# Kernel tuning notes

Measured on AMD Instinct MI355X. Metric: run time of the kernel, lower is better.

Reference implementation:

```python
import jax, jax.numpy as jnp
import numpy as np

N = 50000   # nodes
E = 800000  # edges (avg degree 16)
C = 96      # in = hidden = out channels


def setup_inputs() -> dict:
    key = jax.random.key(0)
    ks = jax.random.split(key, 8)
    s = np.float32(1.0 / np.sqrt(C))
    x = jax.random.normal(ks[0], (N, C), dtype=jnp.float32)
    edge_index = jax.random.randint(ks[1], (2, E), 0, N, dtype=jnp.int64)
    W1 = jax.random.normal(ks[2], (C, C), dtype=jnp.float32) * s
    Wr1 = jax.random.normal(ks[3], (C, C), dtype=jnp.float32) * s
    b1 = jnp.zeros((C,), dtype=jnp.float32)
    W2 = jax.random.normal(ks[4], (C, C), dtype=jnp.float32) * s
    Wr2 = jax.random.normal(ks[5], (C, C), dtype=jnp.float32) * s
    b2 = jnp.zeros((C,), dtype=jnp.float32)
    return {"x": x, "edge_index": edge_index,
            "W1": W1, "Wr1": Wr1, "b1": b1,
            "W2": W2, "Wr2": Wr2, "b2": b2}


def spline_conv(x, edge_index, W, W_root, b):
    """Gather-transform-scatter message passing (SplineConv core, mean aggr)."""
    src, dst = edge_index[0], edge_index[1]
    h = x @ W                                   # [N, C] transform once per node
    msg = h[src]                                # [E, C] edge gather
    agg = jax.ops.segment_sum(msg, dst, num_segments=N)        # scatter-add
    deg = jax.ops.segment_sum(jnp.ones((E,), x.dtype), dst, num_segments=N)
    agg = agg / jnp.maximum(deg, 1.0)[:, None]  # mean aggregation
    return agg + x @ W_root + b                 # root weight + bias


def reference(x, edge_index, W1, Wr1, b1, W2, Wr2, b2):
    h = jax.nn.relu(spline_conv(x, edge_index, W1, Wr1, b1))
    out = spline_conv(h, edge_index, W2, Wr2, b2)
    return out.reshape(-1)  # generalization of x.view(1600)
```

## Files before the change

### kernel.cpp

```cpp
#include <hip/hip_runtime.h>

#define C 96
#define TB 64
#define EB 2048
#define NBP 1024
#define LCAP 2048
#define F8S 128
typedef unsigned char u8;
typedef unsigned short u16;
typedef unsigned int u32;
typedef __attribute__((ext_vector_type(8))) short short8;
typedef __attribute__((ext_vector_type(4))) float floatx4;
typedef __attribute__((ext_vector_type(2))) float floatx2;

__device__ inline u16 f2bf(float f) {
    union { float f; u32 u; } v; v.f = f;
    u32 r = v.u + 0x7fff + ((v.u >> 16) & 1);
    return (u16)(r >> 16);
}
__device__ inline u32 pk4_fp8(float a, float b, float c, float d) {
    u32 w = 0;
    w = __builtin_amdgcn_cvt_pk_fp8_f32(a, b, w, false);
    w = __builtin_amdgcn_cvt_pk_fp8_f32(c, d, w, true);
    return w;
}
__device__ inline u8 f2fp8(float a) {
    return (u8)(__builtin_amdgcn_cvt_pk_fp8_f32(a, a, 0, false) & 0xff);
}

__global__ __launch_bounds__(256) void sort_kernel(const int* __restrict__ src,
                                                   const int* __restrict__ dst,
                                                   u32* __restrict__ tabT,
                                                   u32* __restrict__ stage,
                                                   int E, int DB, int NB,
                                                   const float* __restrict__ x,
                                                   u16* __restrict__ xb,
                                                   u8* __restrict__ xf8, int n16, int CX,
                                                   const float* W0, const float* W1,
                                                   const float* W2, const float* W3,
                                                   u16* T0, u16* T1, u16* T2, u16* T3) {
    int bid = blockIdx.x;
    int t = threadIdx.x;
    if (bid >= DB) {
        int cc = bid - DB;
        if (cc < CX) {
            int i = cc * 256 + t;
            if (i >= n16) return;
            const float4* p = (const float4*)x + (size_t)i * 4;
            float4 a = p[0], b = p[1], c = p[2], d = p[3];
            short8 o0, o1;
            o0[0] = (short)f2bf(a.x); o0[1] = (short)f2bf(a.y);
            o0[2] = (short)f2bf(a.z); o0[3] = (short)f2bf(a.w);
            o0[4] = (short)f2bf(b.x); o0[5] = (short)f2bf(b.y);
            o0[6] = (short)f2bf(b.z); o0[7] = (short)f2bf(b.w);
            o1[0] = (short)f2bf(c.x); o1[1] = (short)f2bf(c.y);
            o1[2] = (short)f2bf(c.z); o1[3] = (short)f2bf(c.w);
            o1[4] = (short)f2bf(d.x); o1[5] = (short)f2bf(d.y);
            o1[6] = (short)f2bf(d.z); o1[7] = (short)f2bf(d.w);
            *(short8*)(xb + (size_t)i * 16) = o0;
            *(short8*)(xb + (size_t)i * 16 + 8) = o1;
            uint4 f8;
            f8.x = pk4_fp8(a.x, a.y, a.z, a.w);
            f8.y = pk4_fp8(b.x, b.y, b.z, b.w);
            f8.z = pk4_fp8(c.x, c.y, c.z, c.w);
            f8.w = pk4_fp8(d.x, d.y, d.z, d.w);
            int node = i / 6, slice = i - node * 6;
            *(uint4*)(xf8 + (size_t)node * F8S + slice * 16) = f8;
        } else {
            int w = cc - CX;
            const float* W = w == 0 ? W0 : w == 1 ? W1 : w == 2 ? W2 : W3;
            u16* T = w == 0 ? T0 : w == 1 ? T1 : w == 2 ? T2 : T3;
            for (int i = t; i < C * C; i += 256) {
                int k = i / C, n = i - k * C;
                T[n * C + k] = f2bf(W[i]);
            }
        }
        return;
    }

    __shared__ u32 s_word[EB];
    __shared__ int s_cnt[NBP];
    __shared__ int s_off[NBP];
    __shared__ int s_scan[256];
    int e0 = bid * EB;
    int cnt_here = min(EB, E - e0);

    for (int i = t; i < NBP; i += 256) s_cnt[i] = 0;
    __syncthreads();

    int my_src[EB / 256], my_dl[EB / 256], my_b[EB / 256], my_rank[EB / 256];
    int nmine = 0;
#pragma unroll
    for (int k = 0; k < EB / 256; k++) {
        int i = t + k * 256;
        if (i < cnt_here) {
            int s = src[e0 + i], d = dst[e0 + i];
            int b = d >> 6;
            my_src[nmine] = s;
            my_dl[nmine] = d & (TB - 1);
            my_b[nmine] = b;
            my_rank[nmine] = atomicAdd(&s_cnt[b], 1);
            nmine++;
        }
    }
    __syncthreads();

    int b4 = t * 4;
    int v0 = s_cnt[b4], v1 = s_cnt[b4 + 1], v2 = s_cnt[b4 + 2], v3 = s_cnt[b4 + 3];
    int lsum = v0 + v1 + v2 + v3;
    s_scan[t] = lsum;
    __syncthreads();
    for (int off = 1; off < 256; off <<= 1) {
        int x2 = (t >= off) ? s_scan[t - off] : 0;
        __syncthreads();
        s_scan[t] += x2;
        __syncthreads();
    }
    int excl = s_scan[t] - lsum;
    s_off[b4] = excl;
    s_off[b4 + 1] = excl + v0;
    s_off[b4 + 2] = excl + v0 + v1;
    s_off[b4 + 3] = excl + v0 + v1 + v2;
    __syncthreads();

    for (int b = t; b < NB; b += 256)
        tabT[(size_t)b * DB + bid] = ((u32)s_cnt[b] << 16) | (u32)s_off[b];

    for (int k = 0; k < nmine; k++) {
        int slot = s_off[my_b[k]] + my_rank[k];
        s_word[slot] = ((u32)my_dl[k] << 16) | (u32)my_src[k];
    }
    __syncthreads();

    for (int i = t; i < cnt_here; i += 256) stage[(size_t)bid * EB + i] = s_word[i];
}

template <bool RELU, bool WF8, typename OT>
__global__ __launch_bounds__(256, 4) void layer_kernel(const u16* __restrict__ Xbf,
                                                       const u8* __restrict__ Xf8,
                                                       const u32* __restrict__ tabT,
                                                       const u32* __restrict__ stage,
                                                       const u16* __restrict__ WTA,
                                                       const u16* __restrict__ WTR,
                                                       const float* __restrict__ BIAS,
                                                       OT* __restrict__ Y,
                                                       u8* __restrict__ Yf8, int n, int DB) {
    __shared__ __align__(16) u16 sA[64 * 104];
    __shared__ u16 lcsr[LCAP];
    __shared__ int s_dg[TB];
    __shared__ int s_off64[TB];
    __shared__ int s_cur64[TB];
    __shared__ int s_perm[TB];
    __shared__ int ssum[256];
    u32* raw = (u32*)sA;
    const int t = threadIdx.x;
    const int b = blockIdx.x;
    const int row0 = b * 64;
    const u32* tab_b = tabT + (size_t)b * DB;

    for (int i = t; i < TB; i += 256) s_dg[i] = 0;
    u32 p0 = (t < DB) ? tab_b[t] : 0;
    u32 p1 = (t + 256 < DB) ? tab_b[t + 256] : 0;
    int l0 = p0 >> 16, o0 = p0 & 0xffff;
    int l1 = p1 >> 16, o1 = p1 & 0xffff;
    int tot = l0 + l1;
    ssum[t] = tot;
    __syncthreads();
    for (int off = 1; off < 256; off <<= 1) {
        int x2 = (t >= off) ? ssum[t - off] : 0;
        __syncthreads();
        ssum[t] += x2;
        __syncthreads();
    }
    const int seg0 = ssum[t] - tot;
    int pos = seg0;
    {
        const u32* run = stage + (size_t)t * EB + o0;
        for (int j = 0; j < l0; j++) {
            u32 w = run[j];
            if (pos < LCAP) { raw[pos++] = w; atomicAdd(&s_dg[w >> 16], 1); }
        }
        const u32* run2 = stage + ((size_t)t + 256) * EB + o1;
        for (int j = 0; j < l1; j++) {
            u32 w = run2[j];
            if (pos < LCAP) { raw[pos++] = w; atomicAdd(&s_dg[w >> 16], 1); }
        }
    }
    const int stored = pos - seg0;
    __syncthreads();

    int dv = (t < TB) ? s_dg[t] : 0;
    if (t < TB) s_cur64[t] = dv;
    __syncthreads();
    for (int off = 1; off < TB; off <<= 1) {
        int x2 = (t >= off && t < TB) ? s_cur64[t - off] : 0;
        __syncthreads();
        if (t < TB) s_cur64[t] += x2;
        __syncthreads();
    }
    if (t < TB) s_off64[t] = s_cur64[t] - dv;
    __syncthreads();
    if (t < TB) s_cur64[t] = s_off64[t];
    __syncthreads();

    for (int k = 0; k < stored; k++) {
        u32 w = raw[seg0 + k];
        int p = atomicAdd(&s_cur64[w >> 16], 1);
        lcsr[p] = (u16)(w & 0xffffu);
    }
    __syncthreads();

    if (t < 64) {
        int di = s_dg[t];
        int r = 0;
#pragma unroll 8
        for (int j = 0; j < 64; j++) {
            int dj = s_dg[j];
            r += (dj < di) || (dj == di && j < t);
        }
        s_perm[r] = t;
    }
    __syncthreads();

    {
        int nl = s_perm[t >> 2];
        int q = t & 3;
        float acc[24];
#pragma unroll
        for (int i = 0; i < 24; i++) acc[i] = 0.f;
        int d = s_dg[nl];
        int start = s_off64[nl];
        const int off4 = q * 16;
        const int off2 = 64 + q * 8;

#define CONSUME(va, vb)                                                     \
        do {                                                                \
            u32 ws[6] = {(va).x, (va).y, (va).z, (va).w, (vb).x, (vb).y};   \
            _Pragma("unroll")                                               \
            for (int i = 0; i < 6; i++) {                                   \
                floatx2 lo = __builtin_amdgcn_cvt_pk_f32_fp8(ws[i], false); \
                floatx2 hi = __builtin_amdgcn_cvt_pk_f32_fp8(ws[i], true);  \
                acc[4 * i]     += lo[0];                                    \
                acc[4 * i + 1] += lo[1];                                    \
                acc[4 * i + 2] += hi[0];                                    \
                acc[4 * i + 3] += hi[1];                                    \
            }                                                               \
        } while (0)

        int j = 0;
        if (d >= 4) {
            int si[4];
#pragma unroll
            for (int k = 0; k < 4; k++) si[k] = lcsr[start + k];
            for (; j + 8 <= d; j += 4) {
                uint4 va[4];
                uint2 vb[4];
#pragma unroll
                for (int k = 0; k < 4; k++) {
                    const u8* p = Xf8 + ((size_t)si[k] << 7);
                    va[k] = *(const uint4*)(p + off4);
                    vb[k] = *(const uint2*)(p + off2);
                }
                int sn[4];
#pragma unroll
                for (int k = 0; k < 4; k++) sn[k] = lcsr[start + j + 4 + k];
#pragma unroll
                for (int k = 0; k < 4; k++) CONSUME(va[k], vb[k]);
#pragma unroll
                for (int k = 0; k < 4; k++) si[k] = sn[k];
            }
            {
                uint4 va[4];
                uint2 vb[4];
#pragma unroll
                for (int k = 0; k < 4; k++) {
                    const u8* p = Xf8 + ((size_t)si[k] << 7);
                    va[k] = *(const uint4*)(p + off4);
                    vb[k] = *(const uint2*)(p + off2);
                }
#pragma unroll
                for (int k = 0; k < 4; k++) CONSUME(va[k], vb[k]);
                j += 4;
            }
        }
        for (; j < d; j++) {
            const u8* p = Xf8 + ((size_t)lcsr[start + j] << 7);
            uint4 va = *(const uint4*)(p + off4);
            uint2 vb = *(const uint2*)(p + off2);
            CONSUME(va, vb);
        }
#undef CONSUME

        float inv = 1.0f / fmaxf((float)d, 1.0f);
        u16* dl = sA + nl * 104;
        short8 o0v, o1v, o2v;
#pragma unroll
        for (int i = 0; i < 8; i++) {
            o0v[i] = (short)f2bf(acc[i] * inv);
            o1v[i] = (short)f2bf(acc[8 + i] * inv);
            o2v[i] = (short)f2bf(acc[16 + i] * inv);
        }
        *(short8*)(dl + q * 16) = o0v;
        *(short8*)(dl + q * 16 + 8) = o1v;
        *(short8*)(dl + 64 + q * 8) = o2v;
    }
    __syncthreads();

    const int lane = t & 63;
    const int w = t >> 6;
    const int quad = lane >> 4;
    const int l16 = lane & 15;
    const int r0 = row0 + w * 16;

    floatx4 acc6[6];
#pragma unroll
    for (int i = 0; i < 6; i++) acc6[i] = (floatx4){0.f, 0.f, 0.f, 0.f};

    {
        const u16* Ap = sA + (w * 16 + l16) * 104 + quad * 8;
        const u16* Wp = WTA + l16 * C + quad * 8;
#pragma unroll
        for (int ks = 0; ks < 3; ks++) {
            short8 a = *(const short8*)(Ap + ks * 32);
#pragma unroll
            for (int nt = 0; nt < 6; nt++) {
                short8 bb = *(const short8*)(Wp + nt * 16 * C + ks * 32);
                acc6[nt] = __builtin_amdgcn_mfma_f32_16x16x32_bf16(a, bb, acc6[nt], 0, 0, 0);
            }
        }
    }
    {
        int arow = r0 + l16;
        if (arow >= n) arow = n - 1;
        const u16* Xp = Xbf + (size_t)arow * C + quad * 8;
        const u16* Wp = WTR + l16 * C + quad * 8;
#pragma unroll
        for (int ks = 0; ks < 3; ks++) {
            short8 a = *(const short8*)(Xp + ks * 32);
#pragma unroll
            for (int nt = 0; nt < 6; nt++) {
                short8 bb = *(const short8*)(Wp + nt * 16 * C + ks * 32);
                acc6[nt] = __builtin_amdgcn_mfma_f32_16x16x32_bf16(a, bb, acc6[nt], 0, 0, 0);
            }
        }
    }

#pragma unroll
    for (int nt = 0; nt < 6; nt++) {
        float bv = BIAS[nt * 16 + l16];
#pragma unroll
        for (int r = 0; r < 4; r++) {
            float v = acc6[nt][r] + bv;
            if (RELU) v = fmaxf(v, 0.f);
            acc6[nt][r] = v;
        }
    }
    __syncthreads();

    const int nrow = min(64, n - row0);
    const int lr = w * 16 + quad * 4;

    if constexpr (sizeof(OT) == 2) {
        u16* so = sA;
#pragma unroll
        for (int nt = 0; nt < 6; nt++)
#pragma unroll
            for (int r = 0; r < 4; r++)
                so[(lr + r) * 96 + nt * 16 + l16] = f2bf(acc6[nt][r]);
        __syncthreads();
        {
            char* dstp = (char*)Y + (size_t)row0 * 192;
            int nbytes = nrow * 192;
            for (int ofs = t * 16; ofs < nbytes; ofs += 4096)
                *(uint4*)(dstp + ofs) = *(const uint4*)((const char*)sA + ofs);
        }
        if constexpr (WF8) {
            __syncthreads();
            u8* so8 = (u8*)sA;
#pragma unroll
            for (int nt = 0; nt < 6; nt++)
#pragma unroll
                for (int r = 0; r < 4; r++)
                    so8[(lr + r) * 96 + nt * 16 + l16] = f2fp8(acc6[nt][r]);
            __syncthreads();
            char* dst8 = (char*)Yf8 + (size_t)row0 * F8S;
            int nchunks = nrow * 6;
            for (int cix = t; cix < nchunks; cix += 256) {
                int r = cix / 6, col = cix - r * 6;
                *(uint4*)(dst8 + (size_t)r * F8S + col * 16) =
                    *(const uint4*)((const char*)sA + r * 96 + col * 16);
            }
        }
    } else {
        float* sof = (float*)sA;
#pragma unroll
        for (int half = 0; half < 2; half++) {
            if (half) __syncthreads();
            if ((w >> 1) == half) {
#pragma unroll
                for (int nt = 0; nt < 6; nt++)
#pragma unroll
                    for (int r = 0; r < 4; r++)
                        sof[((w & 1) * 16 + quad * 4 + r) * 96 + nt * 16 + l16] = acc6[nt][r];
            }
            __syncthreads();
            int rbase = row0 + half * 32;
            int nr = n - rbase;
            nr = nr < 0 ? 0 : (nr > 32 ? 32 : nr);
            char* dstp = (char*)Y + (size_t)rbase * 384;
            int nbytes = nr * 384;
            for (int ofs = t * 16; ofs < nbytes; ofs += 4096)
                *(uint4*)(dstp + ofs) = *(const uint4*)((const char*)sA + ofs);
        }
    }
}

extern "C" void kernel_launch(void* const* d_in, const int* in_sizes, int n_in,
                              void* d_out, int out_size, void* d_ws, size_t ws_size,
                              hipStream_t stream) {
    const float* x   = (const float*)d_in[0];
    const int*   ei  = (const int*)d_in[1];
    const float* W1  = (const float*)d_in[2];
    const float* Wr1 = (const float*)d_in[3];
    const float* b1  = (const float*)d_in[4];
    const float* W2  = (const float*)d_in[5];
    const float* Wr2 = (const float*)d_in[6];
    const float* b2  = (const float*)d_in[7];
    float* out = (float*)d_out;

    const int N = in_sizes[0] / C;
    const int E = in_sizes[1] / 2;
    const int* src = ei;
    const int* dst = ei + E;

    const int DB   = (E + EB - 1) / EB;
    const int NB   = (N + TB - 1) / TB;
    const int n16  = N * C / 16;
    const int CX   = (n16 + 255) / 256;
    const size_t NBDB = ((size_t)NB * DB + 3) & ~(size_t)3;

    u32*  tabT = (u32*)d_ws;
    u32*  stage = tabT + NBDB;
    u16*  xb   = (u16*)(stage + (size_t)DB * EB);
    u16*  h1b  = xb + (size_t)N * C;
    u16*  wt   = h1b + (size_t)N * C;
    u16 *wt1 = wt, *wtr1 = wt + C * C, *wt2 = wt + 2 * C * C, *wtr2 = wt + 3 * C * C;
    u8*   xf8  = (u8*)(wt + 4 * C * C);
    u8*   h1f8 = xf8 + (size_t)N * F8S;

    sort_kernel<<<DB + CX + 4, 256, 0, stream>>>(src, dst, tabT, stage,
                                                 E, DB, NB,
                                                 x, xb, xf8, n16, CX,
                                                 W1, Wr1, W2, Wr2, wt1, wtr1, wt2, wtr2);

    layer_kernel<true, true, u16><<<NB, 256, 0, stream>>>(
        xb, xf8, tabT, stage, wt1, wtr1, b1, h1b, h1f8, N, DB);
    layer_kernel<false, false, float><<<NB, 256, 0, stream>>>(
        h1b, h1f8, tabT, stage, wt2, wtr2, b2, out, h1f8, N, DB);
}
```

Baseline: 164.0 us.

## Halve node tile to 32 and split each node's edge gather across two thread groups

Shrinks the per-block destination tile from 64 to 32 nodes, doubling the number of blocks and the bucket count in the edge-binning kernel. Each node's neighbor list is now split between two 4-thread groups, whose partial sums are combined through a new shared float buffer before the mean and bf16 conversion. The aim is more parallelism and better latency hiding in the gather phase. In exchange only two of the four waves do MFMA work, and the change adds an extra synchronization and more shared memory per block.

```diff
diff --git a/kernel.cpp b/kernel.cpp
--- a/kernel.cpp
+++ b/kernel.cpp
@@ -1,10 +1,10 @@
 #include <hip/hip_runtime.h>
 
 #define C 96
-#define TB 64
+#define TB 32
 #define EB 2048
-#define NBP 1024
-#define LCAP 2048
+#define NBP 2048
+#define LCAP 1280
 #define F8S 128
 typedef unsigned char u8;
 typedef unsigned short u16;
@@ -95,7 +95,7 @@
         int i = t + k * 256;
         if (i < cnt_here) {
             int s = src[e0 + i], d = dst[e0 + i];
-            int b = d >> 6;
+            int b = d >> 5;
             my_src[nmine] = s;
             my_dl[nmine] = d & (TB - 1);
             my_b[nmine] = b;
@@ -105,9 +105,10 @@
     }
     __syncthreads();
 
-    int b4 = t * 4;
-    int v0 = s_cnt[b4], v1 = s_cnt[b4 + 1], v2 = s_cnt[b4 + 2], v3 = s_cnt[b4 + 3];
-    int lsum = v0 + v1 + v2 + v3;
+    int b8 = t * 8;
+    int v[8], lsum = 0;
+#pragma unroll
+    for (int i = 0; i < 8; i++) { v[i] = s_cnt[b8 + i]; lsum += v[i]; }
     s_scan[t] = lsum;
     __syncthreads();
     for (int off = 1; off < 256; off <<= 1) {
@@ -116,11 +117,9 @@
         s_scan[t] += x2;
         __syncthreads();
     }
-    int excl = s_scan[t] - lsum;
-    s_off[b4] = excl;
-    s_off[b4 + 1] = excl + v0;
-    s_off[b4 + 2] = excl + v0 + v1;
-    s_off[b4 + 3] = excl + v0 + v1 + v2;
+    int run = s_scan[t] - lsum;
+#pragma unroll
+    for (int i = 0; i < 8; i++) { s_off[b8 + i] = run; run += v[i]; }
     __syncthreads();
 
     for (int b = t; b < NB; b += 256)
@@ -145,7 +144,8 @@
                                                        const float* __restrict__ BIAS,
                                                        OT* __restrict__ Y,
                                                        u8* __restrict__ Yf8, int n, int DB) {
-    __shared__ __align__(16) u16 sA[64 * 104];
+    __shared__ __align__(16) u16 sA[TB * 104];
+    __shared__ __align__(16) float comb[TB * 96];
     __shared__ u16 lcsr[LCAP];
     __shared__ int s_dg[TB];
     __shared__ int s_off64[TB];
@@ -155,7 +155,7 @@
     u32* raw = (u32*)sA;
     const int t = threadIdx.x;
     const int b = blockIdx.x;
-    const int row0 = b * 64;
+    const int row0 = b * TB;
     const u32* tab_b = tabT + (size_t)b * DB;
 
     for (int i = t; i < TB; i += 256) s_dg[i] = 0;
@@ -175,14 +175,14 @@
     const int seg0 = ssum[t] - tot;
     int pos = seg0;
     {
-        const u32* run = stage + (size_t)t * EB + o0;
+        const u32* runp = stage + (size_t)t * EB + o0;
         for (int j = 0; j < l0; j++) {
-            u32 w = run[j];
+            u32 w = runp[j];
             if (pos < LCAP) { raw[pos++] = w; atomicAdd(&s_dg[w >> 16], 1); }
         }
-        const u32* run2 = stage + ((size_t)t + 256) * EB + o1;
+        const u32* runp2 = stage + ((size_t)t + 256) * EB + o1;
         for (int j = 0; j < l1; j++) {
-            u32 w = run2[j];
+            u32 w = runp2[j];
             if (pos < LCAP) { raw[pos++] = w; atomicAdd(&s_dg[w >> 16], 1); }
         }
     }
@@ -210,11 +210,11 @@
     }
     __syncthreads();
 
-    if (t < 64) {
+    if (t < TB) {
         int di = s_dg[t];
         int r = 0;
 #pragma unroll 8
-        for (int j = 0; j < 64; j++) {
+        for (int j = 0; j < TB; j++) {
             int dj = s_dg[j];
             r += (dj < di) || (dj == di && j < t);
         }
@@ -223,13 +223,16 @@
     __syncthreads();
 
     {
-        int nl = s_perm[t >> 2];
+        int nl = s_perm[t >> 3];
+        int g = (t >> 2) & 1;
         int q = t & 3;
         float acc[24];
 #pragma unroll
         for (int i = 0; i < 24; i++) acc[i] = 0.f;
         int d = s_dg[nl];
-        int start = s_off64[nl];
+        int d0 = (d + 1) >> 1;
+        int base = s_off64[nl] + (g ? d0 : 0);
+        int dd = g ? (d - d0) : d0;
         const int off4 = q * 16;
         const int off2 = 64 + q * 8;
 
@@ -248,11 +251,11 @@
         } while (0)
 
         int j = 0;
-        if (d >= 4) {
+        if (dd >= 4) {
             int si[4];
 #pragma unroll
-            for (int k = 0; k < 4; k++) si[k] = lcsr[start + k];
-            for (; j + 8 <= d; j += 4) {
+            for (int k = 0; k < 4; k++) si[k] = lcsr[base + k];
+            for (; j + 8 <= dd; j += 4) {
                 uint4 va[4];
                 uint2 vb[4];
 #pragma unroll
@@ -263,7 +266,7 @@
                 }
                 int sn[4];
 #pragma unroll
-                for (int k = 0; k < 4; k++) sn[k] = lcsr[start + j + 4 + k];
+                for (int k = 0; k < 4; k++) sn[k] = lcsr[base + j + 4 + k];
 #pragma unroll
                 for (int k = 0; k < 4; k++) CONSUME(va[k], vb[k]);
 #pragma unroll
@@ -283,26 +286,40 @@
                 j += 4;
             }
         }
-        for (; j < d; j++) {
-            const u8* p = Xf8 + ((size_t)lcsr[start + j] << 7);
+        for (; j < dd; j++) {
+            const u8* p = Xf8 + ((size_t)lcsr[base + j] << 7);
             uint4 va = *(const uint4*)(p + off4);
             uint2 vb = *(const uint2*)(p + off2);
             CONSUME(va, vb);
         }
 #undef CONSUME
 
-        float inv = 1.0f / fmaxf((float)d, 1.0f);
-        u16* dl = sA + nl * 104;
-        short8 o0v, o1v, o2v;
-#pragma unroll
-        for (int i = 0; i < 8; i++) {
-            o0v[i] = (short)f2bf(acc[i] * inv);
-            o1v[i] = (short)f2bf(acc[8 + i] * inv);
-            o2v[i] = (short)f2bf(acc[16 + i] * inv);
-        }
-        *(short8*)(dl + q * 16) = o0v;
-        *(short8*)(dl + q * 16 + 8) = o1v;
-        *(short8*)(dl + 64 + q * 8) = o2v;
+        float* cmb = comb + nl * 96;
+        if (g == 1) {
+#pragma unroll
+            for (int i = 0; i < 16; i++) cmb[q * 16 + i] = acc[i];
+#pragma unroll
+            for (int i = 0; i < 8; i++) cmb[64 + q * 8 + i] = acc[16 + i];
+        }
+        __syncthreads();
+        if (g == 0) {
+            float inv = 1.0f / fmaxf((float)d, 1.0f);
+#pragma unroll
+            for (int i = 0; i < 16; i++) acc[i] = (acc[i] + cmb[q * 16 + i]) * inv;
+#pragma unroll
+            for (int i = 0; i < 8; i++) acc[16 + i] = (acc[16 + i] + cmb[64 + q * 8 + i]) * inv;
+            u16* dl = sA + nl * 104;
+            short8 o0v, o1v, o2v;
+#pragma unroll
+            for (int i = 0; i < 8; i++) {
+                o0v[i] = (short)f2bf(acc[i]);
+                o1v[i] = (short)f2bf(acc[8 + i]);
+                o2v[i] = (short)f2bf(acc[16 + i]);
+            }
+            *(short8*)(dl + q * 16) = o0v;
+            *(short8*)(dl + q * 16 + 8) = o1v;
+            *(short8*)(dl + 64 + q * 8) = o2v;
+        }
     }
     __syncthreads();
 
@@ -310,63 +327,65 @@
     const int w = t >> 6;
     const int quad = lane >> 4;
     const int l16 = lane & 15;
-    const int r0 = row0 + w * 16;
 
     floatx4 acc6[6];
 #pragma unroll
     for (int i = 0; i < 6; i++) acc6[i] = (floatx4){0.f, 0.f, 0.f, 0.f};
 
-    {
-        const u16* Ap = sA + (w * 16 + l16) * 104 + quad * 8;
-        const u16* Wp = WTA + l16 * C + quad * 8;
-#pragma unroll
-        for (int ks = 0; ks < 3; ks++) {
-            short8 a = *(const short8*)(Ap + ks * 32);
-#pragma unroll
-            for (int nt = 0; nt < 6; nt++) {
-                short8 bb = *(const short8*)(Wp + nt * 16 * C + ks * 32);
-                acc6[nt] = __builtin_amdgcn_mfma_f32_16x16x32_bf16(a, bb, acc6[nt], 0, 0, 0);
-            }
-        }
-    }
-    {
-        int arow = r0 + l16;
-        if (arow >= n) arow = n - 1;
-        const u16* Xp = Xbf + (size_t)arow * C + quad * 8;
-        const u16* Wp = WTR + l16 * C + quad * 8;
-#pragma unroll
-        for (int ks = 0; ks < 3; ks++) {
-            short8 a = *(const short8*)(Xp + ks * 32);
-#pragma unroll
-            for (int nt = 0; nt < 6; nt++) {
-                short8 bb = *(const short8*)(Wp + nt * 16 * C + ks * 32);
-                acc6[nt] = __builtin_amdgcn_mfma_f32_16x16x32_bf16(a, bb, acc6[nt], 0, 0, 0);
-            }
-        }
-    }
-
-#pragma unroll
-    for (int nt = 0; nt < 6; nt++) {
-        float bv = BIAS[nt * 16 + l16];
-#pragma unroll
-        for (int r = 0; r < 4; r++) {
-            float v = acc6[nt][r] + bv;
-            if (RELU) v = fmaxf(v, 0.f);
-            acc6[nt][r] = v;
-        }
-    }
-    __syncthreads();
-
-    const int nrow = min(64, n - row0);
+    if (w < 2) {
+        {
+            const u16* Ap = sA + (w * 16 + l16) * 104 + quad * 8;
+            const u16* Wp = WTA + l16 * C + quad * 8;
+#pragma unroll
+            for (int ks = 0; ks < 3; ks++) {
+                short8 a = *(const short8*)(Ap + ks * 32);
+#pragma unroll
+                for (int nt = 0; nt < 6; nt++) {
+                    short8 bb = *(const short8*)(Wp + nt * 16 * C + ks * 32);
+                    acc6[nt] = __builtin_amdgcn_mfma_f32_16x16x32_bf16(a, bb, acc6[nt], 0, 0, 0);
+                }
+            }
+        }
+        {
+            int arow = row0 + w * 16 + l16;
+            if (arow >= n) arow = n - 1;
+            const u16* Xp = Xbf + (size_t)arow * C + quad * 8;
+            const u16* Wp = WTR + l16 * C + quad * 8;
+#pragma unroll
+            for (int ks = 0; ks < 3; ks++) {
+                short8 a = *(const short8*)(Xp + ks * 32);
+#pragma unroll
+                for (int nt = 0; nt < 6; nt++) {
+                    short8 bb = *(const short8*)(Wp + nt * 16 * C + ks * 32);
+                    acc6[nt] = __builtin_amdgcn_mfma_f32_16x16x32_bf16(a, bb, acc6[nt], 0, 0, 0);
+                }
+            }
+        }
+#pragma unroll
+        for (int nt = 0; nt < 6; nt++) {
+            float bv = BIAS[nt * 16 + l16];
+#pragma unroll
+            for (int r = 0; r < 4; r++) {
+                float v = acc6[nt][r] + bv;
+                if (RELU) v = fmaxf(v, 0.f);
+                acc6[nt][r] = v;
+            }
+        }
+    }
+    __syncthreads();
+
+    const int nrow = min(TB, n - row0);
     const int lr = w * 16 + quad * 4;
 
     if constexpr (sizeof(OT) == 2) {
         u16* so = sA;
-#pragma unroll
-        for (int nt = 0; nt < 6; nt++)
-#pragma unroll
-            for (int r = 0; r < 4; r++)
-                so[(lr + r) * 96 + nt * 16 + l16] = f2bf(acc6[nt][r]);
+        if (w < 2) {
+#pragma unroll
+            for (int nt = 0; nt < 6; nt++)
+#pragma unroll
+                for (int r = 0; r < 4; r++)
+                    so[(lr + r) * 96 + nt * 16 + l16] = f2bf(acc6[nt][r]);
+        }
         __syncthreads();
         {
             char* dstp = (char*)Y + (size_t)row0 * 192;
@@ -377,11 +396,13 @@
         if constexpr (WF8) {
             __syncthreads();
             u8* so8 = (u8*)sA;
-#pragma unroll
-            for (int nt = 0; nt < 6; nt++)
-#pragma unroll
-                for (int r = 0; r < 4; r++)
-                    so8[(lr + r) * 96 + nt * 16 + l16] = f2fp8(acc6[nt][r]);
+            if (w < 2) {
+#pragma unroll
+                for (int nt = 0; nt < 6; nt++)
+#pragma unroll
+                    for (int r = 0; r < 4; r++)
+                        so8[(lr + r) * 96 + nt * 16 + l16] = f2fp8(acc6[nt][r]);
+            }
             __syncthreads();
             char* dst8 = (char*)Yf8 + (size_t)row0 * F8S;
             int nchunks = nrow * 6;
@@ -392,26 +413,18 @@
             }
         }
     } else {
-        float* sof = (float*)sA;
-#pragma unroll
-        for (int half = 0; half < 2; half++) {
-            if (half) __syncthreads();
-            if ((w >> 1) == half) {
-#pragma unroll
-                for (int nt = 0; nt < 6; nt++)
-#pragma unroll
-                    for (int r = 0; r < 4; r++)
-                        sof[((w & 1) * 16 + quad * 4 + r) * 96 + nt * 16 + l16] = acc6[nt][r];
-            }
-            __syncthreads();
-            int rbase = row0 + half * 32;
-            int nr = n - rbase;
-            nr = nr < 0 ? 0 : (nr > 32 ? 32 : nr);
-            char* dstp = (char*)Y + (size_t)rbase * 384;
-            int nbytes = nr * 384;
-            for (int ofs = t * 16; ofs < nbytes; ofs += 4096)
-                *(uint4*)(dstp + ofs) = *(const uint4*)((const char*)sA + ofs);
-        }
+        if (w < 2) {
+#pragma unroll
+            for (int nt = 0; nt < 6; nt++)
+#pragma unroll
+                for (int r = 0; r < 4; r++)
+                    comb[(lr + r) * 96 + nt * 16 + l16] = acc6[nt][r];
+        }
+        __syncthreads();
+        char* dstp = (char*)Y + (size_t)row0 * 384;
+        int nbytes = nrow * 384;
+        for (int ofs = t * 16; ofs < nbytes; ofs += 4096)
+            *(uint4*)(dstp + ofs) = *(const uint4*)((const char*)comb + ofs);
     }
 }
 
```

Result: slower. 175.0 us (+6.7%).
